# Kernel tuning notes

Hardware: AMD Instinct MI355X
Metric: run time of the kernel (lower is better)

The kernel has to match this reference:

```python
import jax, jax.numpy as jnp
import numpy as np

PAD = 0.1
RESO = 128           # plane_resolution
HID = 128            # hidden_dim
CDIM = 128           # c_dim
NBLK = 5             # n_blocks
PLANES = (('xz', (0, 2)), ('xy', (0, 1)), ('yz', (1, 2)))


def normalize_coordinate(p, dims):
    # p: (B,T,3) -> (B,T,2) in [0, 1)
    xy = p[..., list(dims)] / (1.0 + PAD + 1e-3) + 0.5
    return jnp.clip(xy, 0.0, 1.0 - 1e-5)


def coordinate2index(xy, reso):
    g = (xy * reso).astype(jnp.int32)          # (B,T,2)
    return g[..., 0] + reso * g[..., 1]        # (B,T) flat cell index


def scatter_max_gather(vals, idx, n_cells):
    # vals: (B,T,F), idx: (B,T) -> per-cell max gathered back to points (B,T,F)
    B, T, F = vals.shape
    flat_idx = (idx + jnp.arange(B, dtype=idx.dtype)[:, None] * n_cells).reshape(-1)
    fea = jax.ops.segment_max(vals.reshape(B * T, F), flat_idx, num_segments=B * n_cells)
    return fea[flat_idx].reshape(B, T, F)


def scatter_mean_plane(c, idx, n_cells):
    # c: (B,T,C), idx: (B,T) -> (B, n_cells, C); empty cells stay 0
    B, T, C = c.shape
    flat_idx = (idx + jnp.arange(B, dtype=idx.dtype)[:, None] * n_cells).reshape(-1)
    s = jax.ops.segment_sum(c.reshape(B * T, C), flat_idx, num_segments=B * n_cells)
    cnt = jax.ops.segment_sum(jnp.ones((B * T,), c.dtype), flat_idx, num_segments=B * n_cells)
    return (s / jnp.maximum(cnt, 1.0)[:, None]).reshape(B, n_cells, C)


def resnet_block(x, W0, b0, W1, b1, Ws):
    # ResnetBlockFC(2H -> H), size_h = H, shortcut = Linear(no bias)
    net = jax.nn.relu(x) @ W0 + b0
    dx = jax.nn.relu(net) @ W1 + b1
    return x @ Ws + dx


def setup_inputs() -> dict:
    key = jax.random.key(0)
    ks = jax.random.split(key, 10)
    B, T = 2, 32768
    s = 0.05
    return {
        'p': jax.random.uniform(ks[0], (B, T, 3), jnp.float32, -0.5, 0.5),
        'fc_pos_W': s * jax.random.normal(ks[1], (3, 2 * HID), jnp.float32),
        'fc_pos_b': s * jax.random.normal(ks[2], (2 * HID,), jnp.float32),
        'blocks_W0': s * jax.random.normal(ks[3], (NBLK, 2 * HID, HID), jnp.float32),
        'blocks_b0': s * jax.random.normal(ks[4], (NBLK, HID), jnp.float32),
        'blocks_W1': s * jax.random.normal(ks[5], (NBLK, HID, HID), jnp.float32),
        'blocks_b1': s * jax.random.normal(ks[6], (NBLK, HID), jnp.float32),
        'blocks_Ws': s * jax.random.normal(ks[7], (NBLK, 2 * HID, HID), jnp.float32),
        'fc_c_W': s * jax.random.normal(ks[8], (HID, CDIM), jnp.float32),
        'fc_c_b': s * jax.random.normal(ks[9], (CDIM,), jnp.float32),
    }


def reference(p, fc_pos_W, fc_pos_b, blocks_W0, blocks_b0, blocks_W1, blocks_b1,
              blocks_Ws, fc_c_W, fc_c_b):
    B, T, _ = p.shape
    R2 = RESO * RESO
    index = {k: coordinate2index(normalize_coordinate(p, d), RESO) for k, d in PLANES}

    net = p @ fc_pos_W + fc_pos_b                       # (B,T,2H)
    net = resnet_block(net, blocks_W0[0], blocks_b0[0],
                       blocks_W1[0], blocks_b1[0], blocks_Ws[0])  # (B,T,H)
    for i in range(1, NBLK):
        pooled = sum(scatter_max_gather(net, index[k], R2) for k, _ in PLANES)
        net = jnp.concatenate([net, pooled], axis=-1)   # (B,T,2H)
        net = resnet_block(net, blocks_W0[i], blocks_b0[i],
                           blocks_W1[i], blocks_b1[i], blocks_Ws[i])

    c = net @ fc_c_W + fc_c_b                           # (B,T,C)
    planes = []
    for k, _ in PLANES:  # order: xz, xy, yz
        fea = scatter_mean_plane(c, index[k], R2)       # (B,R2,C)
        planes.append(fea.transpose(0, 2, 1).reshape(B, CDIM, RESO, RESO))
    return jnp.stack(planes)                            # (3,B,C,R,R)
```

## Files before the change

kernel.cpp:

```cpp
#include <hip/hip_runtime.h>

#define TT 65536
#define R2 16384

typedef _Float16 f16x8 __attribute__((ext_vector_type(8)));
typedef float    f32x4 __attribute__((ext_vector_type(4)));
typedef unsigned u32x4 __attribute__((ext_vector_type(4)));

#define MFMA16 __builtin_amdgcn_mfma_f32_16x16x32_f16

__device__ __forceinline__ unsigned short f2h(float f){
    _Float16 h = (_Float16)f;
    return __builtin_bit_cast(unsigned short, h);
}
__device__ __forceinline__ float h2f(unsigned short u){
    return (float)__builtin_bit_cast(_Float16, u);
}
__device__ __forceinline__ unsigned relu2(unsigned w){
    unsigned s = w & 0x80008000u;
    unsigned mask = ((s >> 15) * 0x7FFFu) | s;
    return w & ~mask;
}
__device__ __forceinline__ float nrm(float a){
    float v = a / 1.101f + 0.5f;
    v = fmaxf(v, 0.0f);
    v = fminf(v, 0.99999f);
    return v;
}

__global__ __launch_bounds__(256) void k_repack(const float* __restrict__ W0,
        const float* __restrict__ W1, const float* __restrict__ Ws,
        const float* __restrict__ Wc, unsigned short* __restrict__ out){
    int e = blockIdx.x*256 + threadIdx.x;
    const float* src; int r;
    if (e < 409600){
        int i = e / 81920; r = e % 81920;
        if (r < 32768)      { src = W0 + (size_t)i*32768; }
        else if (r < 49152) { src = W1 + (size_t)i*16384; r -= 32768; }
        else                { src = Ws + (size_t)i*32768; r -= 49152; }
    } else { src = Wc; r = e - 409600; }
    int j = r & 7, l = (r >> 3) & 63, t = (r >> 9) & 7, ks = r >> 12;
    int k = ks*32 + (l >> 4)*8 + j;
    int n = t*16 + (l & 15);
    out[e] = f2h(src[k*128 + n]);
}

__global__ __launch_bounds__(256) void k_idxhist(const float* __restrict__ p,
        int* __restrict__ idx, int* __restrict__ cnt){
    int pt = blockIdx.x*256 + threadIdx.x;
    float p0 = p[pt*3+0], p1 = p[pt*3+1], p2 = p[pt*3+2];
    int g0 = (int)(nrm(p0)*128.f);
    int g1 = (int)(nrm(p1)*128.f);
    int g2 = (int)(nrm(p2)*128.f);
    int i0 = g0 + 128*g2, i1 = g0 + 128*g1, i2 = g1 + 128*g2;
    idx[0*TT + pt] = i0;
    idx[1*TT + pt] = i1;
    idx[2*TT + pt] = i2;
    int b14 = (pt >> 15) << 14;
    atomicAdd(&cnt[0*32768 + b14 + i0], 1);
    atomicAdd(&cnt[1*32768 + b14 + i1], 1);
    atomicAdd(&cnt[2*32768 + b14 + i2], 1);
}

__global__ __launch_bounds__(1024) void k_scan(const int* __restrict__ cnt,
        int* __restrict__ cs, int* __restrict__ cp){
    __shared__ int ls[1024];
    int pl = blockIdx.x, tid = threadIdx.x;
    const int* c = cnt + pl*32768;
    int v[32], tot = 0;
    #pragma unroll
    for (int j = 0; j < 32; j++){ v[j] = c[tid*32 + j]; tot += v[j]; }
    int x = tot;
    ls[tid] = x; __syncthreads();
    for (int off = 1; off < 1024; off <<= 1){
        int add = (tid >= off) ? ls[tid - off] : 0;
        __syncthreads();
        x += add; ls[tid] = x;
        __syncthreads();
    }
    int run = x - tot;
    #pragma unroll
    for (int j = 0; j < 32; j++){
        cs[pl*32769 + tid*32 + j] = run;
        cp[pl*32768 + tid*32 + j] = run;
        run += v[j];
    }
    if (tid == 1023) cs[pl*32769 + 32768] = TT;
}

__global__ __launch_bounds__(256) void k_scatter(const int* __restrict__ idx,
        int* __restrict__ cp, int* __restrict__ srt){
    int pt = blockIdx.x*256 + threadIdx.x;
    int b14 = (pt >> 15) << 14;
    #pragma unroll
    for (int pl = 0; pl < 3; pl++){
        int pos = atomicAdd(&cp[pl*32768 + b14 + idx[pl*TT + pt]], 1);
        srt[pl*TT + pos] = pt;
    }
}

__global__ __launch_bounds__(256) void k_fcpos(const float* __restrict__ p,
        const float* __restrict__ W, const float* __restrict__ b,
        unsigned short* __restrict__ xb){
    int pt = blockIdx.x;
    int j  = threadIdx.x;
    float p0 = p[pt*3+0], p1 = p[pt*3+1], p2 = p[pt*3+2];
    float v = b[j] + p0*W[j] + p1*W[256+j] + p2*W[512+j];
    xb[(size_t)pt*256 + j] = f2h(v);
}

__global__ __launch_bounds__(256) void k_pool3(const unsigned short* __restrict__ xb,
        const int* __restrict__ srt, const int* __restrict__ cs,
        unsigned short* __restrict__ mxp){
    int pl = blockIdx.y;
    const int* srtp = srt + (size_t)pl*TT;
    const int* csp  = cs  + (size_t)pl*32769;
    int lane = threadIdx.x & 63;
    int c = blockIdx.x*4 + (threadIdx.x >> 6);
    int s = csp[c], e = csp[c+1];
    if (s == e) return;
    float m0 = -1e30f, m1 = -1e30f;
    int pt = srtp[s];
    for (int i = s; i < e; i++){
        int ptn = (i+1 < e) ? srtp[i+1] : 0;
        unsigned v = ((const unsigned*)(xb + (size_t)pt*256))[lane];
        m0 = fmaxf(m0, h2f((unsigned short)(v & 0xFFFF)));
        m1 = fmaxf(m1, h2f((unsigned short)(v >> 16)));
        pt = ptn;
    }
    unsigned pk = (unsigned)f2h(m0) | ((unsigned)f2h(m1) << 16);
    ((unsigned*)(mxp + ((size_t)pl*32768 + c)*128))[lane] = pk;
}

__global__ __launch_bounds__(256) void k_resnet(unsigned short* __restrict__ xb,
        const unsigned short* __restrict__ wp,
        const float* __restrict__ b0, const float* __restrict__ b1,
        const int* __restrict__ idx, const unsigned short* __restrict__ mxp){
    __shared__ __align__(16) unsigned short lds[32768];
    unsigned short* lw = lds;
    unsigned short* lt = lds + 16384;
    int tid = threadIdx.x, w = tid >> 6, lane = tid & 63;
    int quad = lane >> 4, l15 = lane & 15;
    int m0 = blockIdx.x*128 + w*32;
    float b0v[8], b1v[8];
    #pragma unroll
    for (int t = 0; t < 8; t++){ b0v[t] = b0[t*16 + l15]; b1v[t] = b1[t*16 + l15]; }

    u32x4 xf[2][4]; f16x8 pf[2][4];
    #pragma unroll
    for (int s = 0; s < 2; s++){
        size_t rb = (size_t)(m0 + s*16 + l15)*256;
        #pragma unroll
        for (int ks = 0; ks < 4; ks++)
            xf[s][ks] = *(const u32x4*)(xb + rb + ks*32 + quad*8);
    }
    if (mxp){
        #pragma unroll
        for (int s = 0; s < 2; s++){
            int row = m0 + s*16 + l15;
            int b14 = (row >> 15) << 14;
            const unsigned short* q0 = mxp + ((size_t)(0*32768 + b14 + idx[row]))*128;
            const unsigned short* q1 = mxp + ((size_t)(1*32768 + b14 + idx[TT + row]))*128;
            const unsigned short* q2 = mxp + ((size_t)(2*32768 + b14 + idx[2*TT + row]))*128;
            #pragma unroll
            for (int ks = 0; ks < 4; ks++){
                int col = ks*32 + quad*8;
                f16x8 a = *(const f16x8*)(q0 + col);
                f16x8 b = *(const f16x8*)(q1 + col);
                f16x8 c = *(const f16x8*)(q2 + col);
                f16x8 r;
                #pragma unroll
                for (int j = 0; j < 8; j++)
                    r[j] = (_Float16)((float)a[j] + (float)b[j] + (float)c[j]);
                pf[s][ks] = r;
            }
        }
    } else {
        #pragma unroll
        for (int s = 0; s < 2; s++){
            size_t rb = (size_t)(m0 + s*16 + l15)*256 + 128;
            #pragma unroll
            for (int ks = 0; ks < 4; ks++)
                pf[s][ks] = *(const f16x8*)(xb + rb + ks*32 + quad*8);
        }
    }

    f32x4 acc[2][8];
    #pragma unroll
    for (int s = 0; s < 2; s++)
        #pragma unroll
        for (int t = 0; t < 8; t++){ f32x4 z = {0.f,0.f,0.f,0.f}; acc[s][t] = z; }

    #pragma unroll
    for (int c = 0; c < 2; c++){
        __syncthreads();
        { const u32x4* g = (const u32x4*)(wp + c*16384); u32x4* l = (u32x4*)lw;
          #pragma unroll
          for (int i = 0; i < 8; i++) l[i*256 + tid] = g[i*256 + tid]; }
        __syncthreads();
        #pragma unroll
        for (int ks = 0; ks < 4; ks++){
            u32x4 u0 = (c == 0) ? xf[0][ks] : __builtin_bit_cast(u32x4, pf[0][ks]);
            u32x4 u1 = (c == 0) ? xf[1][ks] : __builtin_bit_cast(u32x4, pf[1][ks]);
            u0.x = relu2(u0.x); u0.y = relu2(u0.y); u0.z = relu2(u0.z); u0.w = relu2(u0.w);
            u1.x = relu2(u1.x); u1.y = relu2(u1.y); u1.z = relu2(u1.z); u1.w = relu2(u1.w);
            f16x8 a0 = __builtin_bit_cast(f16x8, u0);
            f16x8 a1 = __builtin_bit_cast(f16x8, u1);
            #pragma unroll
            for (int t = 0; t < 8; t++){
                f16x8 b = *(const f16x8*)&lw[((ks*8 + t)*64 + lane)*8];
                acc[0][t] = MFMA16(a0, b, acc[0][t], 0, 0, 0);
                acc[1][t] = MFMA16(a1, b, acc[1][t], 0, 0, 0);
            }
        }
    }

    #pragma unroll
    for (int s = 0; s < 2; s++){
        int strip = w*2 + s;
        #pragma unroll
        for (int t = 0; t < 8; t++){
            int ks2 = t >> 1;
            int l2b = ((t & 1)*2 + ((lane >> 3) & 1))*16 + quad*4;
            #pragma unroll
            for (int r = 0; r < 4; r++){
                float v = acc[s][t][r] + b0v[t];
                v = fmaxf(v, 0.f);
                lt[(((ks2*8 + strip)*64) + l2b + r)*8 + (lane & 7)] = f2h(v);
            }
        }
    }

    __syncthreads();
    { const u32x4* g = (const u32x4*)(wp + 32768); u32x4* l = (u32x4*)lw;
      #pragma unroll
      for (int i = 0; i < 8; i++) l[i*256 + tid] = g[i*256 + tid]; }
    __syncthreads();
    f32x4 acc2[2][8];
    #pragma unroll
    for (int s = 0; s < 2; s++)
        #pragma unroll
        for (int t = 0; t < 8; t++){ f32x4 iv = {b1v[t],b1v[t],b1v[t],b1v[t]}; acc2[s][t] = iv; }
    #pragma unroll
    for (int ks = 0; ks < 4; ks++){
        f16x8 a0 = *(const f16x8*)&lt[((ks*8 + w*2 + 0)*64 + lane)*8];
        f16x8 a1 = *(const f16x8*)&lt[((ks*8 + w*2 + 1)*64 + lane)*8];
        #pragma unroll
        for (int t = 0; t < 8; t++){
            f16x8 b = *(const f16x8*)&lw[((ks*8 + t)*64 + lane)*8];
            acc2[0][t] = MFMA16(a0, b, acc2[0][t], 0, 0, 0);
            acc2[1][t] = MFMA16(a1, b, acc2[1][t], 0, 0, 0);
        }
    }

    #pragma unroll
    for (int c = 0; c < 2; c++){
        __syncthreads();
        { const u32x4* g = (const u32x4*)(wp + 49152 + c*16384); u32x4* l = (u32x4*)lw;
          #pragma unroll
          for (int i = 0; i < 8; i++) l[i*256 + tid] = g[i*256 + tid]; }
        __syncthreads();
        #pragma unroll
        for (int ks = 0; ks < 4; ks++){
            f16x8 a0 = (c == 0) ? __builtin_bit_cast(f16x8, xf[0][ks]) : pf[0][ks];
            f16x8 a1 = (c == 0) ? __builtin_bit_cast(f16x8, xf[1][ks]) : pf[1][ks];
            #pragma unroll
            for (int t = 0; t < 8; t++){
                f16x8 b = *(const f16x8*)&lw[((ks*8 + t)*64 + lane)*8];
                acc2[0][t] = MFMA16(a0, b, acc2[0][t], 0, 0, 0);
                acc2[1][t] = MFMA16(a1, b, acc2[1][t], 0, 0, 0);
            }
        }
    }

    #pragma unroll
    for (int s = 0; s < 2; s++)
        #pragma unroll
        for (int t = 0; t < 8; t++)
            #pragma unroll
            for (int r = 0; r < 4; r++){
                int row = m0 + s*16 + quad*4 + r;
                xb[(size_t)row*256 + t*16 + l15] = f2h(acc2[s][t][r]);
            }
}

__global__ __launch_bounds__(256) void k_fcc(unsigned short* __restrict__ xb,
        const unsigned short* __restrict__ wcp, const float* __restrict__ bc){
    int tid = threadIdx.x, w = tid >> 6, lane = tid & 63;
    int quad = lane >> 4, l15 = lane & 15;
    int m0 = blockIdx.x*128 + w*32;
    float bv[8];
    #pragma unroll
    for (int t = 0; t < 8; t++) bv[t] = bc[t*16 + l15];
    f32x4 acc[2][8];
    #pragma unroll
    for (int s = 0; s < 2; s++)
        #pragma unroll
        for (int t = 0; t < 8; t++){ f32x4 iv = {bv[t],bv[t],bv[t],bv[t]}; acc[s][t] = iv; }
    const size_t row0 = (size_t)(m0 + l15)*256;
    const size_t row1 = row0 + 16*256;
    #pragma unroll
    for (int ks = 0; ks < 4; ks++){
        int ko = ks*32 + quad*8;
        f16x8 a0 = *(const f16x8*)(xb + row0 + ko);
        f16x8 a1 = *(const f16x8*)(xb + row1 + ko);
        #pragma unroll
        for (int t = 0; t < 8; t++){
            f16x8 b = *(const f16x8*)(wcp + ((ks*8 + t)*64 + lane)*8);
            acc[0][t] = MFMA16(a0, b, acc[0][t], 0, 0, 0);
            acc[1][t] = MFMA16(a1, b, acc[1][t], 0, 0, 0);
        }
    }
    #pragma unroll
    for (int s = 0; s < 2; s++)
        #pragma unroll
        for (int t = 0; t < 8; t++)
            #pragma unroll
            for (int r = 0; r < 4; r++){
                int row = m0 + s*16 + quad*4 + r;
                xb[(size_t)row*256 + 128 + t*16 + l15] = f2h(acc[s][t][r]);
            }
}

__global__ __launch_bounds__(1024) void k_psum3(const unsigned short* __restrict__ xb,
        const int* __restrict__ srt, const int* __restrict__ cs,
        float* __restrict__ out){
    __shared__ float ls[32*129];
    int pl = blockIdx.y;
    const int* srtp = srt + (size_t)pl*TT;
    const int* csp  = cs  + (size_t)pl*32769;
    int w = threadIdx.x >> 6, lane = threadIdx.x & 63;
    int c0 = blockIdx.x * 32;
    #pragma unroll
    for (int cc = w; cc < 32; cc += 16){
        int c = c0 + cc;
        int s = csp[c], e = csp[c+1];
        float s0 = 0.f, s1 = 0.f;
        if (s < e){
            int pt = srtp[s];
            for (int i = s; i < e; i++){
                int ptn = (i+1 < e) ? srtp[i+1] : 0;
                unsigned v = ((const unsigned*)(xb + (size_t)pt*256 + 128))[lane];
                s0 += h2f((unsigned short)(v & 0xFFFF));
                s1 += h2f((unsigned short)(v >> 16));
                pt = ptn;
            }
        }
        float rc = (e > s) ? 1.f/(float)(e - s) : 0.f;
        ls[cc*129 + lane*2]     = s0*rc;
        ls[cc*129 + lane*2 + 1] = s1*rc;
    }
    __syncthreads();
    int pb = pl*2 + (c0 >> 14);
    float* o = out + (size_t)pb*128*R2 + (c0 & 16383);
    #pragma unroll
    for (int j = 0; j < 4; j++){
        int lin = j*1024 + threadIdx.x;
        int f = lin >> 5, cc = lin & 31;
        o[(size_t)f*R2 + cc] = ls[cc*129 + f];
    }
}

extern "C" void kernel_launch(void* const* d_in, const int* in_sizes, int n_in,
                              void* d_out, int out_size, void* d_ws, size_t ws_size,
                              hipStream_t stream) {
    const float* p        = (const float*)d_in[0];
    const float* fc_pos_W = (const float*)d_in[1];
    const float* fc_pos_b = (const float*)d_in[2];
    const float* bW0      = (const float*)d_in[3];
    const float* bb0      = (const float*)d_in[4];
    const float* bW1      = (const float*)d_in[5];
    const float* bb1      = (const float*)d_in[6];
    const float* bWs      = (const float*)d_in[7];
    const float* fc_c_W   = (const float*)d_in[8];
    const float* fc_c_b   = (const float*)d_in[9];
    float* out = (float*)d_out;

    char* ws = (char*)d_ws;
    int*            idx   = (int*)ws;
    unsigned short* xbuf  = (unsigned short*)(ws + 786432);
    int*            srt   = (int*)(ws + 34340864);
    int*            cs    = (int*)(ws + 35127296);
    int*            cp    = (int*)(ws + 35520528);
    unsigned short* wpack = (unsigned short*)(ws + 35913744);
    unsigned short* mxp   = (unsigned short*)(ws + 36765712);

    k_repack<<<1664, 256, 0, stream>>>(bW0, bW1, bWs, fc_c_W, wpack);
    hipMemsetAsync(cp, 0, (size_t)3*32768*4, stream);
    k_idxhist<<<TT/256, 256, 0, stream>>>(p, idx, cp);
    k_scan   <<<3, 1024, 0, stream>>>(cp, cs, cp);
    k_scatter<<<TT/256, 256, 0, stream>>>(idx, cp, srt);
    k_fcpos  <<<TT, 256, 0, stream>>>(p, fc_pos_W, fc_pos_b, xbuf);

    k_resnet<<<512, 256, 0, stream>>>(xbuf, wpack, bb0, bb1, idx, (const unsigned short*)nullptr);
    for (int i = 1; i < 5; i++){
        k_pool3<<<dim3(8192, 3), 256, 0, stream>>>(xbuf, srt, cs, mxp);
        k_resnet<<<512, 256, 0, stream>>>(xbuf, wpack + (size_t)i*81920,
                                          bb0 + (size_t)i*128, bb1 + (size_t)i*128,
                                          idx, mxp);
    }

    k_fcc  <<<512, 256, 0, stream>>>(xbuf, wpack + 409600, fc_c_b);
    k_psum3<<<dim3(1024, 3), 1024, 0, stream>>>(xbuf, srt, cs, out);
}
```

Before: 435.3 us.

## Fuse fc_pos and fc_c into resnet kernel and prefetch weights via registers

The fc_pos projection is now computed inside the first resnet kernel straight from point coordinates, and the final fc_c linear layer is fused into the last resnet block's epilogue. This removes two kernel launches and a global round trip of the activation buffer. Weight tiles are prefetched into registers one stage ahead and flushed to LDS between stages, overlapping global loads with MFMA work. The register prefetch buffer and the launch_bounds occupancy hint of 2 add register pressure that could cause spills.

```diff
diff --git a/kernel.cpp b/kernel.cpp
--- a/kernel.cpp
+++ b/kernel.cpp
@@ -97,16 +97,6 @@
         int pos = atomicAdd(&cp[pl*32768 + b14 + idx[pl*TT + pt]], 1);
         srt[pl*TT + pos] = pt;
     }
-}
-
-__global__ __launch_bounds__(256) void k_fcpos(const float* __restrict__ p,
-        const float* __restrict__ W, const float* __restrict__ b,
-        unsigned short* __restrict__ xb){
-    int pt = blockIdx.x;
-    int j  = threadIdx.x;
-    float p0 = p[pt*3+0], p1 = p[pt*3+1], p2 = p[pt*3+2];
-    float v = b[j] + p0*W[j] + p1*W[256+j] + p2*W[512+j];
-    xb[(size_t)pt*256 + j] = f2h(v);
 }
 
 __global__ __launch_bounds__(256) void k_pool3(const unsigned short* __restrict__ xb,
@@ -132,10 +122,13 @@
     ((unsigned*)(mxp + ((size_t)pl*32768 + c)*128))[lane] = pk;
 }
 
-__global__ __launch_bounds__(256) void k_resnet(unsigned short* __restrict__ xb,
+__global__ __launch_bounds__(256, 2) void k_resnet(unsigned short* __restrict__ xb,
         const unsigned short* __restrict__ wp,
         const float* __restrict__ b0, const float* __restrict__ b1,
-        const int* __restrict__ idx, const unsigned short* __restrict__ mxp){
+        const int* __restrict__ idx, const unsigned short* __restrict__ mxp,
+        const float* __restrict__ pin, const float* __restrict__ fW,
+        const float* __restrict__ fb,
+        const unsigned short* __restrict__ wc, const float* __restrict__ bc){
     __shared__ __align__(16) unsigned short lds[32768];
     unsigned short* lw = lds;
     unsigned short* lt = lds + 16384;
@@ -146,15 +139,60 @@
     #pragma unroll
     for (int t = 0; t < 8; t++){ b0v[t] = b0[t*16 + l15]; b1v[t] = b1[t*16 + l15]; }
 
+    u32x4 pre[8];
+    auto preload = [&](const unsigned short* src){
+        const u32x4* g = (const u32x4*)src;
+        #pragma unroll
+        for (int i = 0; i < 8; i++) pre[i] = g[i*256 + tid];
+    };
+    auto flush = [&](){
+        u32x4* l = (u32x4*)lw;
+        #pragma unroll
+        for (int i = 0; i < 8; i++) l[i*256 + tid] = pre[i];
+    };
+
+    preload(wp);
+
     u32x4 xf[2][4]; f16x8 pf[2][4];
-    #pragma unroll
-    for (int s = 0; s < 2; s++){
-        size_t rb = (size_t)(m0 + s*16 + l15)*256;
-        #pragma unroll
-        for (int ks = 0; ks < 4; ks++)
-            xf[s][ks] = *(const u32x4*)(xb + rb + ks*32 + quad*8);
-    }
-    if (mxp){
+    if (pin){
+        #pragma unroll
+        for (int s = 0; s < 2; s++){
+            int row = m0 + s*16 + l15;
+            float p0 = pin[row*3+0], p1 = pin[row*3+1], p2 = pin[row*3+2];
+            #pragma unroll
+            for (int ks = 0; ks < 4; ks++){
+                int c0 = ks*32 + quad*8;
+                unsigned short hx[8], hp[8];
+                #pragma unroll
+                for (int h = 0; h < 2; h++){
+                    f32x4 w0 = *(const f32x4*)(fW + c0 + h*4);
+                    f32x4 w1 = *(const f32x4*)(fW + 256 + c0 + h*4);
+                    f32x4 w2 = *(const f32x4*)(fW + 512 + c0 + h*4);
+                    f32x4 bb = *(const f32x4*)(fb + c0 + h*4);
+                    f32x4 v0 = *(const f32x4*)(fW + 128 + c0 + h*4);
+                    f32x4 v1 = *(const f32x4*)(fW + 384 + c0 + h*4);
+                    f32x4 v2 = *(const f32x4*)(fW + 640 + c0 + h*4);
+                    f32x4 bp = *(const f32x4*)(fb + 128 + c0 + h*4);
+                    #pragma unroll
+                    for (int j = 0; j < 4; j++){
+                        hx[h*4+j] = f2h(bb[j] + p0*w0[j] + p1*w1[j] + p2*w2[j]);
+                        hp[h*4+j] = f2h(bp[j] + p0*v0[j] + p1*v1[j] + p2*v2[j]);
+                    }
+                }
+                unsigned short* dx = (unsigned short*)&xf[s][ks];
+                unsigned short* dp = (unsigned short*)&pf[s][ks];
+                #pragma unroll
+                for (int j = 0; j < 8; j++){ dx[j] = hx[j]; dp[j] = hp[j]; }
+            }
+        }
+    } else {
+        #pragma unroll
+        for (int s = 0; s < 2; s++){
+            size_t rb = (size_t)(m0 + s*16 + l15)*256;
+            #pragma unroll
+            for (int ks = 0; ks < 4; ks++)
+                xf[s][ks] = *(const u32x4*)(xb + rb + ks*32 + quad*8);
+        }
         #pragma unroll
         for (int s = 0; s < 2; s++){
             int row = m0 + s*16 + l15;
@@ -175,14 +213,6 @@
                 pf[s][ks] = r;
             }
         }
-    } else {
-        #pragma unroll
-        for (int s = 0; s < 2; s++){
-            size_t rb = (size_t)(m0 + s*16 + l15)*256 + 128;
-            #pragma unroll
-            for (int ks = 0; ks < 4; ks++)
-                pf[s][ks] = *(const f16x8*)(xb + rb + ks*32 + quad*8);
-        }
     }
 
     f32x4 acc[2][8];
@@ -191,17 +221,12 @@
         #pragma unroll
         for (int t = 0; t < 8; t++){ f32x4 z = {0.f,0.f,0.f,0.f}; acc[s][t] = z; }
 
-    #pragma unroll
-    for (int c = 0; c < 2; c++){
-        __syncthreads();
-        { const u32x4* g = (const u32x4*)(wp + c*16384); u32x4* l = (u32x4*)lw;
-          #pragma unroll
-          for (int i = 0; i < 8; i++) l[i*256 + tid] = g[i*256 + tid]; }
-        __syncthreads();
+    __syncthreads(); flush(); __syncthreads();
+    preload(wp + 16384);
+    {
         #pragma unroll
         for (int ks = 0; ks < 4; ks++){
-            u32x4 u0 = (c == 0) ? xf[0][ks] : __builtin_bit_cast(u32x4, pf[0][ks]);
-            u32x4 u1 = (c == 0) ? xf[1][ks] : __builtin_bit_cast(u32x4, pf[1][ks]);
+            u32x4 u0 = xf[0][ks], u1 = xf[1][ks];
             u0.x = relu2(u0.x); u0.y = relu2(u0.y); u0.z = relu2(u0.z); u0.w = relu2(u0.w);
             u1.x = relu2(u1.x); u1.y = relu2(u1.y); u1.z = relu2(u1.z); u1.w = relu2(u1.w);
             f16x8 a0 = __builtin_bit_cast(f16x8, u0);
@@ -215,6 +240,29 @@
         }
     }
 
+    __syncthreads(); flush(); __syncthreads();
+    preload(wp + 32768);
+    {
+        #pragma unroll
+        for (int ks = 0; ks < 4; ks++){
+            u32x4 u0 = __builtin_bit_cast(u32x4, pf[0][ks]);
+            u32x4 u1 = __builtin_bit_cast(u32x4, pf[1][ks]);
+            u0.x = relu2(u0.x); u0.y = relu2(u0.y); u0.z = relu2(u0.z); u0.w = relu2(u0.w);
+            u1.x = relu2(u1.x); u1.y = relu2(u1.y); u1.z = relu2(u1.z); u1.w = relu2(u1.w);
+            f16x8 a0 = __builtin_bit_cast(f16x8, u0);
+            f16x8 a1 = __builtin_bit_cast(f16x8, u1);
+            #pragma unroll
+            for (int t = 0; t < 8; t++){
+                f16x8 b = *(const f16x8*)&lw[((ks*8 + t)*64 + lane)*8];
+                acc[0][t] = MFMA16(a0, b, acc[0][t], 0, 0, 0);
+                acc[1][t] = MFMA16(a1, b, acc[1][t], 0, 0, 0);
+            }
+        }
+    }
+
+    __syncthreads(); flush(); __syncthreads();
+    preload(wp + 49152);
+    f32x4 acc2[2][8];
     #pragma unroll
     for (int s = 0; s < 2; s++){
         int strip = w*2 + s;
@@ -230,13 +278,6 @@
             }
         }
     }
-
-    __syncthreads();
-    { const u32x4* g = (const u32x4*)(wp + 32768); u32x4* l = (u32x4*)lw;
-      #pragma unroll
-      for (int i = 0; i < 8; i++) l[i*256 + tid] = g[i*256 + tid]; }
-    __syncthreads();
-    f32x4 acc2[2][8];
     #pragma unroll
     for (int s = 0; s < 2; s++)
         #pragma unroll
@@ -253,17 +294,13 @@
         }
     }
 
-    #pragma unroll
-    for (int c = 0; c < 2; c++){
-        __syncthreads();
-        { const u32x4* g = (const u32x4*)(wp + 49152 + c*16384); u32x4* l = (u32x4*)lw;
-          #pragma unroll
-          for (int i = 0; i < 8; i++) l[i*256 + tid] = g[i*256 + tid]; }
-        __syncthreads();
+    __syncthreads(); flush(); __syncthreads();
+    preload(wp + 65536);
+    {
         #pragma unroll
         for (int ks = 0; ks < 4; ks++){
-            f16x8 a0 = (c == 0) ? __builtin_bit_cast(f16x8, xf[0][ks]) : pf[0][ks];
-            f16x8 a1 = (c == 0) ? __builtin_bit_cast(f16x8, xf[1][ks]) : pf[1][ks];
+            f16x8 a0 = __builtin_bit_cast(f16x8, xf[0][ks]);
+            f16x8 a1 = __builtin_bit_cast(f16x8, xf[1][ks]);
             #pragma unroll
             for (int t = 0; t < 8; t++){
                 f16x8 b = *(const f16x8*)&lw[((ks*8 + t)*64 + lane)*8];
@@ -273,6 +310,66 @@
         }
     }
 
+    __syncthreads(); flush(); __syncthreads();
+    if (wc) preload(wc);
+    {
+        #pragma unroll
+        for (int ks = 0; ks < 4; ks++){
+            f16x8 a0 = pf[0][ks];
+            f16x8 a1 = pf[1][ks];
+            #pragma unroll
+            for (int t = 0; t < 8; t++){
+                f16x8 b = *(const f16x8*)&lw[((ks*8 + t)*64 + lane)*8];
+                acc2[0][t] = MFMA16(a0, b, acc2[0][t], 0, 0, 0);
+                acc2[1][t] = MFMA16(a1, b, acc2[1][t], 0, 0, 0);
+            }
+        }
+    }
+
+    if (!wc){
+        #pragma unroll
+        for (int s = 0; s < 2; s++)
+            #pragma unroll
+            for (int t = 0; t < 8; t++)
+                #pragma unroll
+                for (int r = 0; r < 4; r++){
+                    int row = m0 + s*16 + quad*4 + r;
+                    xb[(size_t)row*256 + t*16 + l15] = f2h(acc2[s][t][r]);
+                }
+        return;
+    }
+
+    __syncthreads(); flush(); __syncthreads();
+    #pragma unroll
+    for (int s = 0; s < 2; s++){
+        int strip = w*2 + s;
+        #pragma unroll
+        for (int t = 0; t < 8; t++){
+            int ks2 = t >> 1;
+            int l2b = ((t & 1)*2 + ((lane >> 3) & 1))*16 + quad*4;
+            #pragma unroll
+            for (int r = 0; r < 4; r++)
+                lt[(((ks2*8 + strip)*64) + l2b + r)*8 + (lane & 7)] = f2h(acc2[s][t][r]);
+        }
+    }
+    f32x4 acc3[2][8];
+    #pragma unroll
+    for (int t = 0; t < 8; t++){
+        float bv = bc[t*16 + l15];
+        f32x4 iv = {bv, bv, bv, bv};
+        acc3[0][t] = iv; acc3[1][t] = iv;
+    }
+    #pragma unroll
+    for (int ks = 0; ks < 4; ks++){
+        f16x8 a0 = *(const f16x8*)&lt[((ks*8 + w*2 + 0)*64 + lane)*8];
+        f16x8 a1 = *(const f16x8*)&lt[((ks*8 + w*2 + 1)*64 + lane)*8];
+        #pragma unroll
+        for (int t = 0; t < 8; t++){
+            f16x8 b = *(const f16x8*)&lw[((ks*8 + t)*64 + lane)*8];
+            acc3[0][t] = MFMA16(a0, b, acc3[0][t], 0, 0, 0);
+            acc3[1][t] = MFMA16(a1, b, acc3[1][t], 0, 0, 0);
+        }
+    }
     #pragma unroll
     for (int s = 0; s < 2; s++)
         #pragma unroll
@@ -280,45 +377,7 @@
             #pragma unroll
             for (int r = 0; r < 4; r++){
                 int row = m0 + s*16 + quad*4 + r;
-                xb[(size_t)row*256 + t*16 + l15] = f2h(acc2[s][t][r]);
-            }
-}
-
-__global__ __launch_bounds__(256) void k_fcc(unsigned short* __restrict__ xb,
-        const unsigned short* __restrict__ wcp, const float* __restrict__ bc){
-    int tid = threadIdx.x, w = tid >> 6, lane = tid & 63;
-    int quad = lane >> 4, l15 = lane & 15;
-    int m0 = blockIdx.x*128 + w*32;
-    float bv[8];
-    #pragma unroll
-    for (int t = 0; t < 8; t++) bv[t] = bc[t*16 + l15];
-    f32x4 acc[2][8];
-    #pragma unroll
-    for (int s = 0; s < 2; s++)
-        #pragma unroll
-        for (int t = 0; t < 8; t++){ f32x4 iv = {bv[t],bv[t],bv[t],bv[t]}; acc[s][t] = iv; }
-    const size_t row0 = (size_t)(m0 + l15)*256;
-    const size_t row1 = row0 + 16*256;
-    #pragma unroll
-    for (int ks = 0; ks < 4; ks++){
-        int ko = ks*32 + quad*8;
-        f16x8 a0 = *(const f16x8*)(xb + row0 + ko);
-        f16x8 a1 = *(const f16x8*)(xb + row1 + ko);
-        #pragma unroll
-        for (int t = 0; t < 8; t++){
-            f16x8 b = *(const f16x8*)(wcp + ((ks*8 + t)*64 + lane)*8);
-            acc[0][t] = MFMA16(a0, b, acc[0][t], 0, 0, 0);
-            acc[1][t] = MFMA16(a1, b, acc[1][t], 0, 0, 0);
-        }
-    }
-    #pragma unroll
-    for (int s = 0; s < 2; s++)
-        #pragma unroll
-        for (int t = 0; t < 8; t++)
-            #pragma unroll
-            for (int r = 0; r < 4; r++){
-                int row = m0 + s*16 + quad*4 + r;
-                xb[(size_t)row*256 + 128 + t*16 + l15] = f2h(acc[s][t][r]);
+                xb[(size_t)row*256 + 128 + t*16 + l15] = f2h(acc3[s][t][r]);
             }
 }
 
@@ -390,16 +449,22 @@
     k_idxhist<<<TT/256, 256, 0, stream>>>(p, idx, cp);
     k_scan   <<<3, 1024, 0, stream>>>(cp, cs, cp);
     k_scatter<<<TT/256, 256, 0, stream>>>(idx, cp, srt);
-    k_fcpos  <<<TT, 256, 0, stream>>>(p, fc_pos_W, fc_pos_b, xbuf);
-
-    k_resnet<<<512, 256, 0, stream>>>(xbuf, wpack, bb0, bb1, idx, (const unsigned short*)nullptr);
+
+    k_resnet<<<512, 256, 0, stream>>>(xbuf, wpack, bb0, bb1,
+            idx, (const unsigned short*)nullptr,
+            p, fc_pos_W, fc_pos_b,
+            (const unsigned short*)nullptr, (const float*)nullptr);
+
     for (int i = 1; i < 5; i++){
         k_pool3<<<dim3(8192, 3), 256, 0, stream>>>(xbuf, srt, cs, mxp);
+        const unsigned short* wc = (i == 4) ? (wpack + 409600) : (const unsigned short*)nullptr;
+        const float* bcp = (i == 4) ? fc_c_b : (const float*)nullptr;
         k_resnet<<<512, 256, 0, stream>>>(xbuf, wpack + (size_t)i*81920,
-                                          bb0 + (size_t)i*128, bb1 + (size_t)i*128,
-                                          idx, mxp);
-    }
-
-    k_fcc  <<<512, 256, 0, stream>>>(xbuf, wpack + 409600, fc_c_b);
+                bb0 + (size_t)i*128, bb1 + (size_t)i*128,
+                idx, mxp,
+                (const float*)nullptr, (const float*)nullptr, (const float*)nullptr,
+                wc, bcp);
+    }
+
     k_psum3<<<dim3(1024, 3), 1024, 0, stream>>>(xbuf, srt, cs, out);
 }
```

After: 412.8 us. 5.2% less time.
